# Kernel optimization log

Hardware: AMD Instinct MI355X
Metric: run time of the kernel (lower is better)

## Reference

```python
import jax, jax.numpy as jnp
import numpy as np

KNOTS = 16
BN_EPS = 1e-5  # flax BatchNorm default


def _normalize_spline_params(W, H, D):
    # widths/heights sum to 1 over the [0,1] hypercube; slopes positive
    dx = jax.nn.softmax(W, axis=-1)          # (N, d, K) bin widths
    dy = jax.nn.softmax(H, axis=-1)          # (N, d, K) bin heights
    sl = jax.nn.softplus(D)                  # (N, d, K-1) interior knot slopes
    return dx, dy, sl


def _gather_bin(a, idx):
    # a: (N, d, K'), idx: (N, d) -> (N, d)
    return jnp.take_along_axis(a, idx[..., None], axis=-1)[..., 0]


def _rqs_forward(t, dx, dy, sl):
    """Rational-quadratic spline on [0,1] (Durkan et al. 2019); identity outside.
    t: (N, d); dx, dy: (N, d, K); sl: (N, d, K-1).
    Returns y: (N, d), log_det: (N,)."""
    K = dx.shape[-1]
    zero = jnp.zeros_like(dx[..., :1])
    one = jnp.ones_like(dx[..., :1])
    xk = jnp.concatenate([zero, jnp.cumsum(dx, axis=-1)], axis=-1)   # (N, d, K+1) knot x
    yk = jnp.concatenate([zero, jnp.cumsum(dy, axis=-1)], axis=-1)   # (N, d, K+1) knot y
    dk = jnp.concatenate([one, sl, one], axis=-1)                    # (N, d, K+1) knot slopes

    in_bounds = (t >= 0.0) & (t <= 1.0)
    tc = jnp.clip(t, 0.0, 1.0)
    # per-element bin search (vectorized searchsorted)
    idx = jnp.clip(jnp.sum((tc[..., None] >= xk).astype(jnp.int32), axis=-1) - 1, 0, K - 1)

    xk_b = _gather_bin(xk, idx)
    yk_b = _gather_bin(yk, idx)
    dx_b = _gather_bin(dx, idx)
    dy_b = _gather_bin(dy, idx)
    d0 = _gather_bin(dk, idx)
    d1 = _gather_bin(dk, idx + 1)

    xi = (tc - xk_b) / dx_b            # position within bin, in [0,1]
    s = dy_b / dx_b                    # bin mean slope
    xi1m = xi * (1.0 - xi)
    den = s + (d0 + d1 - 2.0 * s) * xi1m
    y_in = yk_b + dy_b * (s * xi * xi + d0 * xi1m) / den
    dydx = s * s * (d1 * xi * xi + 2.0 * s * xi1m + d0 * (1.0 - xi) ** 2) / (den * den)

    y = jnp.where(in_bounds, y_in, t)
    log_det = jnp.sum(jnp.where(in_bounds, jnp.log(dydx), 0.0), axis=1)  # (N,)
    return y, log_det


def setup_inputs() -> dict:
    key = jax.random.key(0)
    ks = jax.random.split(key, 8)
    N, D, C = 65536, 64, 16
    d = D // 2
    spline_dim = 3 * KNOTS - 1
    cin = d + C           # conditioner input width: hstack(xc, c)
    H1, H2 = 128, 128     # layers=(128,128)

    def dense(k, fi, fo):
        return (jax.random.normal(k, (fi, fo), jnp.float32) / np.float32(np.sqrt(fi)))

    return {
        "x": jax.random.uniform(ks[0], (N, D), jnp.float32),
        "c": jax.random.normal(ks[1], (N, C), jnp.float32),
        "bn_scale": jnp.ones((cin,), jnp.float32),
        "bn_bias": jnp.zeros((cin,), jnp.float32),
        "bn_mean": 0.1 * jax.random.normal(ks[2], (cin,), jnp.float32),
        "bn_var": jax.random.uniform(ks[3], (cin,), jnp.float32, minval=0.5, maxval=1.5),
        "W0": dense(ks[4], cin, H1), "b0": jnp.zeros((H1,), jnp.float32),
        "W1": dense(ks[5], H1, H2), "b1": jnp.zeros((H2,), jnp.float32),
        "W2": dense(ks[6], H2, d * spline_dim), "b2": jnp.zeros((d * spline_dim,), jnp.float32),
    }


def reference(x, c, bn_scale, bn_bias, bn_mean, bn_var, W0, b0, W1, b1, W2, b2):
    N, D = x.shape
    d = D // 2
    xt, xc = x[:, :d], x[:, d:]
    h = jnp.hstack((xc, c))
    # BatchNorm in eval mode (use_running_average=True)
    h = (h - bn_mean) * jax.lax.rsqrt(bn_var + BN_EPS) * bn_scale + bn_bias
    h = jax.nn.swish(h @ W0 + b0)
    h = jax.nn.swish(h @ W1 + b1)
    p = (h @ W2 + b2).reshape(N, d, 3 * KNOTS - 1)
    dx, dy, sl = _normalize_spline_params(
        p[..., :KNOTS], p[..., KNOTS:2 * KNOTS], p[..., 2 * KNOTS:])
    yt, log_det = _rqs_forward(xt, dx, dy, sl)
    y = jnp.hstack((yt, xc))
    return y, log_det
```

## Files before the change

### kernel.cpp

```cpp
#include <hip/hip_runtime.h>
#include <math.h>

#define BN_EPS 1e-5f
#define ROWS 64

typedef __attribute__((ext_vector_type(8))) short short8;
typedef __attribute__((ext_vector_type(4))) float float4v;

__device__ __forceinline__ unsigned short f2bf(float f) {
    union { float f; unsigned int u; } v; v.f = f;
    unsigned int r = v.u + 0x7FFF + ((v.u >> 16) & 1);
    return (unsigned short)(r >> 16);
}
__device__ __forceinline__ float softplus_f(float v) {
    float e = __expf(-fabsf(v));
    float r = __logf(1.f + e);
    return v > 0.f ? v + r : r;
}
__device__ __forceinline__ float swish_f(float a) {
    return a / (1.f + __expf(-a));
}

__device__ __forceinline__ float max16(const float* p) {
    float a = fmaxf(p[0], p[1]),  b = fmaxf(p[2], p[3]);
    float c = fmaxf(p[4], p[5]),  d = fmaxf(p[6], p[7]);
    float e = fmaxf(p[8], p[9]),  f = fmaxf(p[10], p[11]);
    float g = fmaxf(p[12], p[13]), h = fmaxf(p[14], p[15]);
    a = fmaxf(a, b); c = fmaxf(c, d); e = fmaxf(e, f); g = fmaxf(g, h);
    return fmaxf(fmaxf(a, c), fmaxf(e, g));
}

#define PREP_WIDE_THREADS (1536 * 128 + 128 * 128)
__global__ void prep_weights(const float* __restrict__ W0, const float* __restrict__ W1,
                             const float* __restrict__ W2, const float* __restrict__ b0,
                             const float* __restrict__ b2,
                             const float* __restrict__ bn_scale, const float* __restrict__ bn_bias,
                             const float* __restrict__ bn_mean, const float* __restrict__ bn_var,
                             unsigned short* __restrict__ Wt0, unsigned short* __restrict__ Wt1,
                             unsigned short* __restrict__ Wt2, float* __restrict__ b0p,
                             float* __restrict__ b2p) {
    const int bid = blockIdx.x, tid = threadIdx.x;
    if (bid < 832) {
        int i = bid * 256 + tid;
        if (i < 1536 * 128) {
            int k = i / 1536, colp = i - k * 1536;
            int dd = colp / 48, j = colp - dd * 48;
            float v = (j < 47) ? W2[k * 1504 + dd * 47 + j] : 0.f;
            Wt2[(size_t)colp * 128 + k] = f2bf(v);
        } else {
            int i2 = i - 1536 * 128;
            int k = i2 >> 7, n = i2 & 127;
            Wt1[n * 128 + k] = f2bf(W1[k * 128 + n]);
        }
        return;
    }
    if (bid == 832) {
        __shared__ float lds[48 * 129 + 96];
        float* a   = lds + 48 * 129;
        float* bsh = a + 48;
        if (tid < 48) {
            float av = bn_scale[tid] * rsqrtf(bn_var[tid] + BN_EPS);
            a[tid] = av;
            bsh[tid] = bn_bias[tid] - bn_mean[tid] * av;
        }
        for (int idx = tid; idx < 48 * 128; idx += 256) {
            int k = idx >> 7, n = idx & 127;
            lds[k * 129 + n] = W0[k * 128 + n];
        }
        __syncthreads();
        #pragma unroll 4
        for (int it = 0; it < 32; ++it) {
            int n = (tid >> 6) + it * 4;
            int k = tid & 63;
            float v = (k < 48) ? lds[k * 129 + n] * a[k] : 0.f;
            Wt0[n * 64 + k] = f2bf(v);
        }
        if (tid < 128) {
            float s = b0[tid];
            #pragma unroll
            for (int k = 0; k < 48; ++k) s += bsh[k] * lds[k * 129 + tid];
            b0p[tid] = s;
        }
        return;
    }
    for (int e = tid; e < 32 * 48; e += 256) {
        int dd = e / 48, j = e - dd * 48;
        b2p[e] = (j < 47) ? b2[dd * 47 + j] : 0.f;
    }
}

__launch_bounds__(256, 4)
__global__ void nsc_mfma(const float* __restrict__ x, const float* __restrict__ c,
                         const unsigned short* __restrict__ Wt0, const float* __restrict__ b0p,
                         const unsigned short* __restrict__ Wt1, const float* __restrict__ b1,
                         const unsigned short* __restrict__ Wt2, const float* __restrict__ b2p,
                         float* __restrict__ out, int N) {
    __shared__ __align__(16) char smem[38912];
    unsigned short* h0 = (unsigned short*)smem;
    unsigned short* h2 = (unsigned short*)smem;
    unsigned short* h1 = (unsigned short*)(smem + 17408);
    float*          ldp = (float*)(smem + 17408 + 20480);

    const int tid  = threadIdx.x;
    const int lane = tid & 63;
    const int l    = lane & 15;
    const int q    = lane >> 4;
    const int wu   = __builtin_amdgcn_readfirstlane(tid >> 6);
    const int r0   = blockIdx.x * ROWS;
    float* pw = (float*)(smem + 17408) + wu * (64 * 20);

    for (int idx = tid; idx < 64 * 64; idx += 256) {
        int r = idx >> 6, j = idx & 63;
        float h = 0.f;
        if (j < 48) {
            int row = r0 + r;
            h = (j < 32) ? x[(size_t)row * 64 + 32 + j] : c[(size_t)row * 16 + (j - 32)];
        }
        h0[r * 72 + j] = f2bf(h);
    }
    for (int idx = tid; idx < 64 * 8; idx += 256) {
        int r = idx >> 3, ch = idx & 7;
        float4v v = *(const float4v*)(x + (size_t)(r0 + r) * 64 + 32 + ch * 4);
        *(float4v*)(out + (size_t)(r0 + r) * 64 + 32 + ch * 4) = v;
    }
    __syncthreads();

    {
        float4v acc[2][4];
        float4v z = {0.f, 0.f, 0.f, 0.f};
        #pragma unroll
        for (int nt = 0; nt < 2; ++nt)
            #pragma unroll
            for (int mt = 0; mt < 4; ++mt) acc[nt][mt] = z;
        #pragma unroll
        for (int ks = 0; ks < 2; ++ks) {
            short8 a[4];
            #pragma unroll
            for (int mt = 0; mt < 4; ++mt)
                a[mt] = *(const short8*)(h0 + (mt * 16 + l) * 72 + ks * 32 + (q << 3));
            #pragma unroll
            for (int nt = 0; nt < 2; ++nt) {
                int n0 = (wu * 2 + nt) * 16;
                short8 b = *(const short8*)(Wt0 + (n0 + l) * 64 + ks * 32 + (q << 3));
                #pragma unroll
                for (int mt = 0; mt < 4; ++mt)
                    acc[nt][mt] = __builtin_amdgcn_mfma_f32_16x16x32_bf16(a[mt], b, acc[nt][mt], 0, 0, 0);
            }
        }
        #pragma unroll
        for (int nt = 0; nt < 2; ++nt) {
            int n0 = (wu * 2 + nt) * 16;
            float bb = b0p[n0 + l];
            #pragma unroll
            for (int mt = 0; mt < 4; ++mt)
                #pragma unroll
                for (int r = 0; r < 4; ++r)
                    h1[(mt * 16 + q * 4 + r) * 136 + n0 + l] = f2bf(swish_f(acc[nt][mt][r] + bb));
        }
    }
    __syncthreads();

    {
        float4v acc[2][4];
        float4v z = {0.f, 0.f, 0.f, 0.f};
        #pragma unroll
        for (int nt = 0; nt < 2; ++nt)
            #pragma unroll
            for (int mt = 0; mt < 4; ++mt) acc[nt][mt] = z;
        #pragma unroll
        for (int ks = 0; ks < 4; ++ks) {
            short8 a[4];
            #pragma unroll
            for (int mt = 0; mt < 4; ++mt)
                a[mt] = *(const short8*)(h1 + (mt * 16 + l) * 136 + ks * 32 + (q << 3));
            #pragma unroll
            for (int nt = 0; nt < 2; ++nt) {
                int n0 = (wu * 2 + nt) * 16;
                short8 b = *(const short8*)(Wt1 + (n0 + l) * 128 + ks * 32 + (q << 3));
                #pragma unroll
                for (int mt = 0; mt < 4; ++mt)
                    acc[nt][mt] = __builtin_amdgcn_mfma_f32_16x16x32_bf16(a[mt], b, acc[nt][mt], 0, 0, 0);
            }
        }
        #pragma unroll
        for (int nt = 0; nt < 2; ++nt) {
            int n0 = (wu * 2 + nt) * 16;
            float bb = b1[n0 + l];
            #pragma unroll
            for (int mt = 0; mt < 4; ++mt)
                #pragma unroll
                for (int r = 0; r < 4; ++r)
                    h2[(mt * 16 + q * 4 + r) * 136 + n0 + l] = f2bf(swish_f(acc[nt][mt][r] + bb));
        }
    }
    __syncthreads();

    float ld_local = 0.f;
    float yreg[8];
    for (int pass = 0; pass < 8; ++pass) {
        const int d = wu * 8 + pass;
        float t = x[(size_t)(r0 + lane) * 64 + d];
        float4v bj0 = *(const float4v*)(b2p + d * 48 +      (q << 2));
        float4v bj1 = *(const float4v*)(b2p + d * 48 + 16 + (q << 2));
        float4v bj2 = *(const float4v*)(b2p + d * 48 + 32 + (q << 2));
        bool inb = (t >= 0.f) && (t <= 1.f);
        float tc = fminf(fmaxf(t, 0.f), 1.f);

        float4v acc[3][4];
        float4v z = {0.f, 0.f, 0.f, 0.f};
        #pragma unroll
        for (int jt = 0; jt < 3; ++jt)
            #pragma unroll
            for (int smt = 0; smt < 4; ++smt) acc[jt][smt] = z;
        __builtin_amdgcn_s_setprio(1);
        #pragma unroll
        for (int ks = 0; ks < 4; ++ks) {
            short8 bf[4];
            #pragma unroll
            for (int smt = 0; smt < 4; ++smt)
                bf[smt] = *(const short8*)(h2 + (smt * 16 + l) * 136 + ks * 32 + (q << 3));
            #pragma unroll
            for (int jt = 0; jt < 3; ++jt) {
                short8 a = *(const short8*)(Wt2 + (size_t)(d * 48 + jt * 16 + l) * 128 + ks * 32 + (q << 3));
                #pragma unroll
                for (int smt = 0; smt < 4; ++smt)
                    acc[jt][smt] = __builtin_amdgcn_mfma_f32_16x16x32_bf16(a, bf[smt], acc[jt][smt], 0, 0, 0);
            }
        }
        __builtin_amdgcn_s_setprio(0);

        float prW[16], prH[16];
        #pragma unroll
        for (int smt = 0; smt < 4; ++smt)
            *(float4v*)(pw + (smt * 16 + l) * 20 + (q << 2)) = acc[0][smt] + bj0;
        #pragma unroll
        for (int c2 = 0; c2 < 4; ++c2)
            *(float4v*)(prW + c2 * 4) = *(const float4v*)(pw + lane * 20 + c2 * 4);
        #pragma unroll
        for (int smt = 0; smt < 4; ++smt)
            *(float4v*)(pw + (smt * 16 + l) * 20 + (q << 2)) = acc[1][smt] + bj1;
        #pragma unroll
        for (int c2 = 0; c2 < 4; ++c2)
            *(float4v*)(prH + c2 * 4) = *(const float4v*)(pw + lane * 20 + c2 * 4);
        #pragma unroll
        for (int smt = 0; smt < 4; ++smt)
            *(float4v*)(pw + (smt * 16 + l) * 20 + (q << 2)) = acc[2][smt] + bj2;

        float mW = max16(prW);
        #pragma unroll
        for (int i = 0; i < 16; ++i) prW[i] = __expf(prW[i] - mW);
        float pw0 = prW[0] + prW[1],   pw1 = prW[2] + prW[3];
        float pw2 = prW[4] + prW[5],   pw3 = prW[6] + prW[7];
        float pw4 = prW[8] + prW[9],   pw5 = prW[10] + prW[11];
        float pw6 = prW[12] + prW[13], pw7 = prW[14] + prW[15];
        float qw0 = pw0 + pw1, qw1 = pw2 + pw3, qw2 = pw4 + pw5, qw3 = pw6 + pw7;
        float ow0 = qw0 + qw1, ow1 = qw2 + qw3;
        float sW = ow0 + ow1;
        float ts = tc * sW;
        bool b3 = (ts >= ow0);
        float base = b3 ? ow0 : 0.f;
        float qsel = b3 ? qw2 : qw0;
        bool b2 = (ts >= base + qsel);
        base += b2 ? qsel : 0.f;
        float psel = b2 ? (b3 ? pw6 : pw2) : (b3 ? pw4 : pw0);
        bool b1 = (ts >= base + psel);
        base += b1 ? psel : 0.f;
        float eev = b1 ? (b2 ? (b3 ? prW[14] : prW[6]) : (b3 ? prW[10] : prW[2]))
                       : (b2 ? (b3 ? prW[12] : prW[4]) : (b3 ? prW[8]  : prW[0]));
        bool b0 = (ts >= base + eev);
        base += b0 ? eev : 0.f;
        float eod = b1 ? (b2 ? (b3 ? prW[15] : prW[7]) : (b3 ? prW[11] : prW[3]))
                       : (b2 ? (b3 ? prW[13] : prW[5]) : (b3 ? prW[9]  : prW[1]));
        float xkb = base;
        float dxb = b0 ? eod : eev;
        int idx = (b3 ? 8 : 0) + (b2 ? 4 : 0) + (b1 ? 2 : 0) + (b0 ? 1 : 0);

        int i0 = (idx > 0)  ? idx - 1 : 0;
        int i1 = (idx < 15) ? idx     : 14;
        float pa0 = pw[lane * 20 + i0];
        float pa1 = pw[lane * 20 + i1];

        float mH = max16(prH);
        #pragma unroll
        for (int i = 0; i < 16; ++i) prH[i] = __expf(prH[i] - mH);
        float ph0 = prH[0] + prH[1],   ph1 = prH[2] + prH[3];
        float ph2 = prH[4] + prH[5],   ph3 = prH[6] + prH[7];
        float ph4 = prH[8] + prH[9],   ph5 = prH[10] + prH[11];
        float ph6 = prH[12] + prH[13], ph7 = prH[14] + prH[15];
        float qh0 = ph0 + ph1, qh1 = ph2 + ph3, qh2 = ph4 + ph5, qh3 = ph6 + ph7;
        float oh0 = qh0 + qh1, oh1 = qh2 + qh3;
        float sH = oh0 + oh1;
        float invH = 1.f / sH;
        float qhsel = b3 ? qh2 : qh0;
        float phsel = b2 ? (b3 ? ph6 : ph2) : (b3 ? ph4 : ph0);
        float ehev = b1 ? (b2 ? (b3 ? prH[14] : prH[6]) : (b3 ? prH[10] : prH[2]))
                        : (b2 ? (b3 ? prH[12] : prH[4]) : (b3 ? prH[8]  : prH[0]));
        float ehod = b1 ? (b2 ? (b3 ? prH[15] : prH[7]) : (b3 ? prH[11] : prH[3]))
                        : (b2 ? (b3 ? prH[13] : prH[5]) : (b3 ? prH[9]  : prH[1]));
        float ykb = (b3 ? oh0 : 0.f) + (b2 ? qhsel : 0.f) +
                    (b1 ? phsel : 0.f) + (b0 ? ehev : 0.f);
        float dyb = b0 ? ehod : ehev;

        float d0 = (idx == 0)  ? 1.f : softplus_f(pa0);
        float d1 = (idx == 15) ? 1.f : softplus_f(pa1);

        float rdx = 1.f / dxb;
        float xi  = (ts - xkb) * rdx;
        float dyn = dyb * invH;
        float ykn = ykb * invH;
        float s   = dyn * sW * rdx;
        float xim = 1.f - xi;
        float x1m = xi * xim;
        float den = s + (d0 + d1 - 2.f * s) * x1m;
        float rden = 1.f / den;
        float y_in = ykn + dyn * (s * xi * xi + d0 * x1m) * rden;
        float dydx = s * s * (d1 * xi * xi + 2.f * s * x1m + d0 * xim * xim) * (rden * rden);

        yreg[pass] = inb ? y_in : t;
        ld_local += inb ? __logf(dydx) : 0.f;
    }

    {
        float4v* o = (float4v*)(out + (size_t)(r0 + lane) * 64 + wu * 8);
        o[0] = *(const float4v*)(yreg);
        o[1] = *(const float4v*)(yreg + 4);
    }
    ldp[wu * 64 + lane] = ld_local;
    __syncthreads();
    if (tid < 64) {
        out[(size_t)N * 64 + r0 + tid] =
            ldp[tid] + ldp[64 + tid] + ldp[128 + tid] + ldp[192 + tid];
    }
}

extern "C" void kernel_launch(void* const* d_in, const int* in_sizes, int n_in,
                              void* d_out, int out_size, void* d_ws, size_t ws_size,
                              hipStream_t stream) {
    const float* x        = (const float*)d_in[0];
    const float* c        = (const float*)d_in[1];
    const float* bn_scale = (const float*)d_in[2];
    const float* bn_bias  = (const float*)d_in[3];
    const float* bn_mean  = (const float*)d_in[4];
    const float* bn_var   = (const float*)d_in[5];
    const float* W0       = (const float*)d_in[6];
    const float* b0       = (const float*)d_in[7];
    const float* W1       = (const float*)d_in[8];
    const float* b1       = (const float*)d_in[9];
    const float* W2       = (const float*)d_in[10];
    const float* b2       = (const float*)d_in[11];
    float* out = (float*)d_out;

    unsigned short* Wt0 = (unsigned short*)d_ws;
    unsigned short* Wt1 = Wt0 + 128 * 64;
    unsigned short* Wt2 = Wt1 + 128 * 128;
    float*          b2p = (float*)(Wt2 + 1536 * 128);
    float*          b0p = b2p + 32 * 48;

    const int N = in_sizes[0] / 64;
    prep_weights<<<834, 256, 0, stream>>>(W0, W1, W2, b0, b2,
                                          bn_scale, bn_bias, bn_mean, bn_var,
                                          Wt0, Wt1, Wt2, b0p, b2p);
    nsc_mfma<<<N / ROWS, 256, 0, stream>>>(x, c, Wt0, b0p, Wt1, b1, Wt2, b2p, out, N);
}
```

Before: 164.0 us.

## Shrink blocks to 32 rows and 2 waves, each wave handling two spline dims

Halves the row tile per block to 32 and uses two waves instead of four. Each wave now computes wider N-tiles in the first two GEMMs and two output dimensions per pass in the final GEMM, packing both halves' epilogues into a 64-lane layout. The aim is more, smaller blocks for better occupancy and latency hiding, with lower LDS use per block. In exchange, each wave does more MFMA work with more accumulator registers, and Wt2 traffic per row doubles relative to the 64-row tile.

```diff
diff --git a/kernel.cpp b/kernel.cpp
--- a/kernel.cpp
+++ b/kernel.cpp
@@ -2,7 +2,7 @@
 #include <math.h>
 
 #define BN_EPS 1e-5f
-#define ROWS 64
+#define ROWS 32
 
 typedef __attribute__((ext_vector_type(8))) short short8;
 typedef __attribute__((ext_vector_type(4))) float float4v;
@@ -89,17 +89,17 @@
     }
 }
 
-__launch_bounds__(256, 4)
+__launch_bounds__(128, 4)
 __global__ void nsc_mfma(const float* __restrict__ x, const float* __restrict__ c,
                          const unsigned short* __restrict__ Wt0, const float* __restrict__ b0p,
                          const unsigned short* __restrict__ Wt1, const float* __restrict__ b1,
                          const unsigned short* __restrict__ Wt2, const float* __restrict__ b2p,
                          float* __restrict__ out, int N) {
-    __shared__ __align__(16) char smem[38912];
+    __shared__ __align__(16) char smem[19456];
     unsigned short* h0 = (unsigned short*)smem;
     unsigned short* h2 = (unsigned short*)smem;
-    unsigned short* h1 = (unsigned short*)(smem + 17408);
-    float*          ldp = (float*)(smem + 17408 + 20480);
+    unsigned short* h1 = (unsigned short*)(smem + 8704);
+    float*          ldp = (float*)(smem + 8704 + 10240);
 
     const int tid  = threadIdx.x;
     const int lane = tid & 63;
@@ -107,9 +107,9 @@
     const int q    = lane >> 4;
     const int wu   = __builtin_amdgcn_readfirstlane(tid >> 6);
     const int r0   = blockIdx.x * ROWS;
-    float* pw = (float*)(smem + 17408) + wu * (64 * 20);
-
-    for (int idx = tid; idx < 64 * 64; idx += 256) {
+    float* pw = (float*)(smem + 8704) + wu * (64 * 20);
+
+    for (int idx = tid; idx < 32 * 64; idx += 128) {
         int r = idx >> 6, j = idx & 63;
         float h = 0.f;
         if (j < 48) {
@@ -118,7 +118,7 @@
         }
         h0[r * 72 + j] = f2bf(h);
     }
-    for (int idx = tid; idx < 64 * 8; idx += 256) {
+    for (int idx = tid; idx < 32 * 8; idx += 128) {
         int r = idx >> 3, ch = idx & 7;
         float4v v = *(const float4v*)(x + (size_t)(r0 + r) * 64 + 32 + ch * 4);
         *(float4v*)(out + (size_t)(r0 + r) * 64 + 32 + ch * 4) = v;
@@ -126,33 +126,33 @@
     __syncthreads();
 
     {
-        float4v acc[2][4];
+        float4v acc[4][2];
         float4v z = {0.f, 0.f, 0.f, 0.f};
         #pragma unroll
-        for (int nt = 0; nt < 2; ++nt)
-            #pragma unroll
-            for (int mt = 0; mt < 4; ++mt) acc[nt][mt] = z;
+        for (int nt = 0; nt < 4; ++nt)
+            #pragma unroll
+            for (int mt = 0; mt < 2; ++mt) acc[nt][mt] = z;
         #pragma unroll
         for (int ks = 0; ks < 2; ++ks) {
-            short8 a[4];
-            #pragma unroll
-            for (int mt = 0; mt < 4; ++mt)
+            short8 a[2];
+            #pragma unroll
+            for (int mt = 0; mt < 2; ++mt)
                 a[mt] = *(const short8*)(h0 + (mt * 16 + l) * 72 + ks * 32 + (q << 3));
             #pragma unroll
-            for (int nt = 0; nt < 2; ++nt) {
-                int n0 = (wu * 2 + nt) * 16;
+            for (int nt = 0; nt < 4; ++nt) {
+                int n0 = (wu * 4 + nt) * 16;
                 short8 b = *(const short8*)(Wt0 + (n0 + l) * 64 + ks * 32 + (q << 3));
                 #pragma unroll
-                for (int mt = 0; mt < 4; ++mt)
+                for (int mt = 0; mt < 2; ++mt)
                     acc[nt][mt] = __builtin_amdgcn_mfma_f32_16x16x32_bf16(a[mt], b, acc[nt][mt], 0, 0, 0);
             }
         }
         #pragma unroll
-        for (int nt = 0; nt < 2; ++nt) {
-            int n0 = (wu * 2 + nt) * 16;
+        for (int nt = 0; nt < 4; ++nt) {
+            int n0 = (wu * 4 + nt) * 16;
             float bb = b0p[n0 + l];
             #pragma unroll
-            for (int mt = 0; mt < 4; ++mt)
+            for (int mt = 0; mt < 2; ++mt)
                 #pragma unroll
                 for (int r = 0; r < 4; ++r)
                     h1[(mt * 16 + q * 4 + r) * 136 + n0 + l] = f2bf(swish_f(acc[nt][mt][r] + bb));
@@ -161,33 +161,33 @@
     __syncthreads();
 
     {
-        float4v acc[2][4];
+        float4v acc[4][2];
         float4v z = {0.f, 0.f, 0.f, 0.f};
         #pragma unroll
-        for (int nt = 0; nt < 2; ++nt)
-            #pragma unroll
-            for (int mt = 0; mt < 4; ++mt) acc[nt][mt] = z;
+        for (int nt = 0; nt < 4; ++nt)
+            #pragma unroll
+            for (int mt = 0; mt < 2; ++mt) acc[nt][mt] = z;
         #pragma unroll
         for (int ks = 0; ks < 4; ++ks) {
-            short8 a[4];
-            #pragma unroll
-            for (int mt = 0; mt < 4; ++mt)
+            short8 a[2];
+            #pragma unroll
+            for (int mt = 0; mt < 2; ++mt)
                 a[mt] = *(const short8*)(h1 + (mt * 16 + l) * 136 + ks * 32 + (q << 3));
             #pragma unroll
-            for (int nt = 0; nt < 2; ++nt) {
-                int n0 = (wu * 2 + nt) * 16;
+            for (int nt = 0; nt < 4; ++nt) {
+                int n0 = (wu * 4 + nt) * 16;
                 short8 b = *(const short8*)(Wt1 + (n0 + l) * 128 + ks * 32 + (q << 3));
                 #pragma unroll
-                for (int mt = 0; mt < 4; ++mt)
+                for (int mt = 0; mt < 2; ++mt)
                     acc[nt][mt] = __builtin_amdgcn_mfma_f32_16x16x32_bf16(a[mt], b, acc[nt][mt], 0, 0, 0);
             }
         }
         #pragma unroll
-        for (int nt = 0; nt < 2; ++nt) {
-            int n0 = (wu * 2 + nt) * 16;
+        for (int nt = 0; nt < 4; ++nt) {
+            int n0 = (wu * 4 + nt) * 16;
             float bb = b1[n0 + l];
             #pragma unroll
-            for (int mt = 0; mt < 4; ++mt)
+            for (int mt = 0; mt < 2; ++mt)
                 #pragma unroll
                 for (int r = 0; r < 4; ++r)
                     h2[(mt * 16 + q * 4 + r) * 136 + n0 + l] = f2bf(swish_f(acc[nt][mt][r] + bb));
@@ -195,56 +195,72 @@
     }
     __syncthreads();
 
+    const int half = lane >> 5;
+    const int row  = lane & 31;
     float ld_local = 0.f;
     float yreg[8];
     for (int pass = 0; pass < 8; ++pass) {
-        const int d = wu * 8 + pass;
-        float t = x[(size_t)(r0 + lane) * 64 + d];
-        float4v bj0 = *(const float4v*)(b2p + d * 48 +      (q << 2));
-        float4v bj1 = *(const float4v*)(b2p + d * 48 + 16 + (q << 2));
-        float4v bj2 = *(const float4v*)(b2p + d * 48 + 32 + (q << 2));
+        const int d0 = wu * 16 + pass;
+        const int d1 = d0 + 8;
+        const int dme = half ? d1 : d0;
+        float t = x[(size_t)(r0 + row) * 64 + dme];
+        float4v bj00 = *(const float4v*)(b2p + d0 * 48 +      (q << 2));
+        float4v bj01 = *(const float4v*)(b2p + d0 * 48 + 16 + (q << 2));
+        float4v bj02 = *(const float4v*)(b2p + d0 * 48 + 32 + (q << 2));
+        float4v bj10 = *(const float4v*)(b2p + d1 * 48 +      (q << 2));
+        float4v bj11 = *(const float4v*)(b2p + d1 * 48 + 16 + (q << 2));
+        float4v bj12 = *(const float4v*)(b2p + d1 * 48 + 32 + (q << 2));
         bool inb = (t >= 0.f) && (t <= 1.f);
         float tc = fminf(fmaxf(t, 0.f), 1.f);
 
-        float4v acc[3][4];
+        float4v acc0[3][2], acc1[3][2];
         float4v z = {0.f, 0.f, 0.f, 0.f};
         #pragma unroll
         for (int jt = 0; jt < 3; ++jt)
             #pragma unroll
-            for (int smt = 0; smt < 4; ++smt) acc[jt][smt] = z;
+            for (int smt = 0; smt < 2; ++smt) { acc0[jt][smt] = z; acc1[jt][smt] = z; }
         __builtin_amdgcn_s_setprio(1);
         #pragma unroll
         for (int ks = 0; ks < 4; ++ks) {
-            short8 bf[4];
-            #pragma unroll
-            for (int smt = 0; smt < 4; ++smt)
+            short8 bf[2];
+            #pragma unroll
+            for (int smt = 0; smt < 2; ++smt)
                 bf[smt] = *(const short8*)(h2 + (smt * 16 + l) * 136 + ks * 32 + (q << 3));
             #pragma unroll
             for (int jt = 0; jt < 3; ++jt) {
-                short8 a = *(const short8*)(Wt2 + (size_t)(d * 48 + jt * 16 + l) * 128 + ks * 32 + (q << 3));
-                #pragma unroll
-                for (int smt = 0; smt < 4; ++smt)
-                    acc[jt][smt] = __builtin_amdgcn_mfma_f32_16x16x32_bf16(a, bf[smt], acc[jt][smt], 0, 0, 0);
+                short8 a0 = *(const short8*)(Wt2 + (size_t)(d0 * 48 + jt * 16 + l) * 128 + ks * 32 + (q << 3));
+                short8 a1 = *(const short8*)(Wt2 + (size_t)(d1 * 48 + jt * 16 + l) * 128 + ks * 32 + (q << 3));
+                #pragma unroll
+                for (int smt = 0; smt < 2; ++smt) {
+                    acc0[jt][smt] = __builtin_amdgcn_mfma_f32_16x16x32_bf16(a0, bf[smt], acc0[jt][smt], 0, 0, 0);
+                    acc1[jt][smt] = __builtin_amdgcn_mfma_f32_16x16x32_bf16(a1, bf[smt], acc1[jt][smt], 0, 0, 0);
+                }
             }
         }
         __builtin_amdgcn_s_setprio(0);
 
         float prW[16], prH[16];
         #pragma unroll
-        for (int smt = 0; smt < 4; ++smt)
-            *(float4v*)(pw + (smt * 16 + l) * 20 + (q << 2)) = acc[0][smt] + bj0;
+        for (int smt = 0; smt < 2; ++smt) {
+            *(float4v*)(pw + (smt * 16 + l) * 20 + (q << 2))        = acc0[0][smt] + bj00;
+            *(float4v*)(pw + (32 + smt * 16 + l) * 20 + (q << 2))   = acc1[0][smt] + bj10;
+        }
         #pragma unroll
         for (int c2 = 0; c2 < 4; ++c2)
             *(float4v*)(prW + c2 * 4) = *(const float4v*)(pw + lane * 20 + c2 * 4);
         #pragma unroll
-        for (int smt = 0; smt < 4; ++smt)
-            *(float4v*)(pw + (smt * 16 + l) * 20 + (q << 2)) = acc[1][smt] + bj1;
+        for (int smt = 0; smt < 2; ++smt) {
+            *(float4v*)(pw + (smt * 16 + l) * 20 + (q << 2))        = acc0[1][smt] + bj01;
+            *(float4v*)(pw + (32 + smt * 16 + l) * 20 + (q << 2))   = acc1[1][smt] + bj11;
+        }
         #pragma unroll
         for (int c2 = 0; c2 < 4; ++c2)
             *(float4v*)(prH + c2 * 4) = *(const float4v*)(pw + lane * 20 + c2 * 4);
         #pragma unroll
-        for (int smt = 0; smt < 4; ++smt)
-            *(float4v*)(pw + (smt * 16 + l) * 20 + (q << 2)) = acc[2][smt] + bj2;
+        for (int smt = 0; smt < 2; ++smt) {
+            *(float4v*)(pw + (smt * 16 + l) * 20 + (q << 2))        = acc0[2][smt] + bj02;
+            *(float4v*)(pw + (32 + smt * 16 + l) * 20 + (q << 2))   = acc1[2][smt] + bj12;
+        }
 
         float mW = max16(prW);
         #pragma unroll
@@ -301,8 +317,8 @@
                     (b1 ? phsel : 0.f) + (b0 ? ehev : 0.f);
         float dyb = b0 ? ehod : ehev;
 
-        float d0 = (idx == 0)  ? 1.f : softplus_f(pa0);
-        float d1 = (idx == 15) ? 1.f : softplus_f(pa1);
+        float d0s = (idx == 0)  ? 1.f : softplus_f(pa0);
+        float d1s = (idx == 15) ? 1.f : softplus_f(pa1);
 
         float rdx = 1.f / dxb;
         float xi  = (ts - xkb) * rdx;
@@ -311,25 +327,25 @@
         float s   = dyn * sW * rdx;
         float xim = 1.f - xi;
         float x1m = xi * xim;
-        float den = s + (d0 + d1 - 2.f * s) * x1m;
+        float den = s + (d0s + d1s - 2.f * s) * x1m;
         float rden = 1.f / den;
-        float y_in = ykn + dyn * (s * xi * xi + d0 * x1m) * rden;
-        float dydx = s * s * (d1 * xi * xi + 2.f * s * x1m + d0 * xim * xim) * (rden * rden);
+        float y_in = ykn + dyn * (s * xi * xi + d0s * x1m) * rden;
+        float dydx = s * s * (d1s * xi * xi + 2.f * s * x1m + d0s * xim * xim) * (rden * rden);
 
         yreg[pass] = inb ? y_in : t;
         ld_local += inb ? __logf(dydx) : 0.f;
     }
 
     {
-        float4v* o = (float4v*)(out + (size_t)(r0 + lane) * 64 + wu * 8);
+        float4v* o = (float4v*)(out + (size_t)(r0 + row) * 64 + wu * 16 + half * 8);
         o[0] = *(const float4v*)(yreg);
         o[1] = *(const float4v*)(yreg + 4);
     }
-    ldp[wu * 64 + lane] = ld_local;
+    ldp[(wu * 2 + half) * 32 + row] = ld_local;
     __syncthreads();
-    if (tid < 64) {
+    if (tid < 32) {
         out[(size_t)N * 64 + r0 + tid] =
-            ldp[tid] + ldp[64 + tid] + ldp[128 + tid] + ldp[192 + tid];
+            ldp[tid] + ldp[32 + tid] + ldp[64 + tid] + ldp[96 + tid];
     }
 }
 
@@ -360,5 +376,5 @@
     prep_weights<<<834, 256, 0, stream>>>(W0, W1, W2, b0, b2,
                                           bn_scale, bn_bias, bn_mean, bn_var,
                                           Wt0, Wt1, Wt2, b0p, b2p);
-    nsc_mfma<<<N / ROWS, 256, 0, stream>>>(x, c, Wt0, b0p, Wt1, b1, Wt2, b2p, out, N);
-}
+    nsc_mfma<<<N / ROWS, 128, 0, stream>>>(x, c, Wt0, b0p, Wt1, b1, Wt2, b2p, out, N);
+}
```

New measurement: 209.8 us. +27.9%, slower.
